# Kernel optimization log

Measured on AMD Instinct MI355X. Metric: run time of the kernel, lower is better.

## Reference

```python
import jax, jax.numpy as jnp
import numpy as np

B, T, I, E, H = 128, 64, 128, 256, 512


def setup_inputs() -> dict:
    key = jax.random.key(0)
    ks = jax.random.split(key, 8)
    inp = {}
    inp["input_data"] = jax.random.normal(ks[0], (B, T, I, E), dtype=jnp.float32)
    inp["news_W"] = jax.random.normal(ks[1], (1, E), dtype=jnp.float32) / np.sqrt(E)
    inp["news_b"] = jnp.zeros((1,), dtype=jnp.float32)
    inp["attn1_W"] = jax.random.normal(ks[2], (T, 2 * H), dtype=jnp.float32) / np.sqrt(2 * H)
    inp["attn1_b"] = jnp.zeros((T,), dtype=jnp.float32)
    inp["attn2_W"] = jax.random.normal(ks[3], (T, T), dtype=jnp.float32) / np.sqrt(T)
    inp["attn2_b"] = jnp.zeros((T,), dtype=jnp.float32)
    inp["attn3_W"] = jax.random.normal(ks[4], (1, T), dtype=jnp.float32) / np.sqrt(T)
    inp["attn3_b"] = jnp.zeros((1,), dtype=jnp.float32)
    inp["W_ih"] = jax.random.normal(ks[5], (4 * H, I), dtype=jnp.float32) / np.sqrt(I)
    inp["W_hh"] = jax.random.normal(ks[6], (4 * H, H), dtype=jnp.float32) / np.sqrt(H)
    inp["b_ih"] = jnp.zeros((4 * H,), dtype=jnp.float32)
    inp["b_hh"] = jnp.zeros((4 * H,), dtype=jnp.float32)
    return inp


def reference(input_data, news_W, news_b, attn1_W, attn1_b, attn2_W, attn2_b,
              attn3_W, attn3_b, W_ih, W_hh, b_ih, b_hh):
    # news_linear: [B,T,I,E] -> [B,T,I]
    x = jnp.einsum('btie,e->bti', input_data, news_W[0]) + news_b[0]
    # z2 is loop-invariant: attn2 on [B,I,T] -> [B,I,T]
    z2 = jnp.einsum('bit,st->bis', x.transpose(0, 2, 1), attn2_W) + attn2_b
    h0 = jnp.zeros((B, H), dtype=x.dtype)
    c0 = jnp.zeros((B, H), dtype=x.dtype)

    def step(carry, x_t):
        h, c = carry
        # hidden/cell repeated across I -> z1 identical for every driver i
        hc = jnp.concatenate([h, c], axis=-1)                   # [B,2H]
        z1 = hc @ attn1_W.T + attn1_b                           # [B,T]
        s = jnp.tanh(z1[:, None, :] + z2)                       # [B,I,T]
        z3 = jnp.einsum('bit,t->bi', s, attn3_W[0]) + attn3_b[0]  # [B,I]
        attn = jax.nn.softmax(z3, axis=1)                       # [B,I]
        w = attn * x_t                                          # [B,I]
        gates = w @ W_ih.T + h @ W_hh.T + b_ih + b_hh           # [B,4H]
        i_g, f_g, g_g, o_g = jnp.split(gates, 4, axis=-1)
        c_new = jax.nn.sigmoid(f_g) * c + jax.nn.sigmoid(i_g) * jnp.tanh(g_g)
        h_new = jax.nn.sigmoid(o_g) * jnp.tanh(c_new)
        return (h_new, c_new), h_new

    xs = x.transpose(1, 0, 2)                                   # [T,B,I]
    _, hs = jax.lax.scan(step, (h0, c0), xs)                    # [T,B,H]
    return hs.transpose(1, 0, 2)                                # [B,T,H]
```

## Files before the change

kernel.cpp:

```cpp
#include <hip/hip_runtime.h>
#include <cstdint>
#include <cstddef>

#define B 128
#define T 64
#define IDIM 128
#define E 256
#define H 512
#define NT 512

#define AT_STRIDE 34
#define AT_CH (128 * AT_STRIDE)

#define OFF_W   0
#define OFF_A   20480
#define OFF_HC  (OFF_A + 4 * AT_CH)
#define OFF_Z1  (OFF_HC + 1024)
#define OFF_RED (OFF_Z1 + 64)
#define OFF_BI  (OFF_RED + 128)
#define POOL_F  (OFF_BI + 32)

__device__ __forceinline__ float waveReduceSum(float v) {
    for (int off = 32; off > 0; off >>= 1) v += __shfl_xor(v, off, 64);
    return v;
}

__device__ __forceinline__ float fast_tanh(float v) {
    float a = fabsf(v);
    float e = __expf(-2.f * a);
    float r = (1.f - e) * __builtin_amdgcn_rcpf(1.f + e);
    return copysignf(r, v);
}

__device__ __forceinline__ float sigmoidf_(float x) {
    return 1.0f / (1.0f + __expf(-x));
}

__device__ __forceinline__ float aload(const float* p) {
    return __hip_atomic_load(p, __ATOMIC_RELAXED, __HIP_MEMORY_SCOPE_AGENT);
}
__device__ __forceinline__ void astore(float* p, float v) {
    __hip_atomic_store(p, v, __ATOMIC_RELAXED, __HIP_MEMORY_SCOPE_AGENT);
}

__device__ __forceinline__ float4 cload4(const float* p) {
    float4 v;
    asm volatile("global_load_dwordx4 %0, %1, off sc0 sc1" : "=v"(v) : "v"(p));
    return v;
}
__device__ __forceinline__ void waitvm0() {
    asm volatile("s_waitcnt vmcnt(0)" ::: "memory");
}

__global__ __launch_bounds__(256) void news_kernel(
    const float* __restrict__ in, const float* __restrict__ nW,
    const float* __restrict__ nb, float* __restrict__ x)
{
    int out_idx = blockIdx.x * 4 + (threadIdx.x >> 6);
    int lane = threadIdx.x & 63;
    const float4* src = (const float4*)(in + (size_t)out_idx * E);
    float4 a = src[lane];
    float4 wv = ((const float4*)nW)[lane];
    float s = a.x * wv.x + a.y * wv.y + a.z * wv.z + a.w * wv.w;
    s = waveReduceSum(s);
    if (lane == 0) x[out_idx] = s + nb[0];
}

__global__ __launch_bounds__(64) void z2_kernel(
    const float* __restrict__ x, const float* __restrict__ A2,
    const float* __restrict__ b2, float* __restrict__ z2)
{
    int b = blockIdx.x >> 7;
    int i = blockIdx.x & 127;
    int s = threadIdx.x;
    __shared__ float xs[T];
    xs[s] = x[((size_t)b * T + s) * IDIM + i];
    __syncthreads();
    float acc = b2[s];
    const float* arow = A2 + s * T;
#pragma unroll 8
    for (int tt = 0; tt < T; ++tt) acc += xs[tt] * arow[tt];
    z2[((size_t)b * IDIM + i) * T + s] = acc;
}

__device__ __forceinline__ void qarrive(int* cnt, int q, int ns, int ph) {
    __syncthreads();
    if (threadIdx.x == NT - 1) {
        asm volatile("s_waitcnt vmcnt(0) lgkmcnt(0)" ::: "memory");
        int* subp  = cnt + (q * 8 + (ns >> 3)) * 32;
        int* rootp = cnt + 1024 + q * 32;
        int old = __hip_atomic_fetch_add(subp, 1, __ATOMIC_RELAXED,
                                         __HIP_MEMORY_SCOPE_AGENT);
        if (old == ph * 8 - 1)
            __hip_atomic_fetch_add(rootp, 1, __ATOMIC_RELAXED,
                                   __HIP_MEMORY_SCOPE_AGENT);
    }
}
__device__ __forceinline__ void qwait(int* cnt, int q, int ph) {
    if (threadIdx.x == NT - 1) {
        int* rootp = cnt + 1024 + q * 32;
        int spins = 0;
        while (__hip_atomic_load(rootp, __ATOMIC_RELAXED,
                                 __HIP_MEMORY_SCOPE_AGENT) < ph * 8) {
            if (++spins > (1 << 16)) break;
        }
    }
    __syncthreads();
}

__global__ __launch_bounds__(NT, 1) void scan_kernel(
    const float* __restrict__ x, const float* __restrict__ z2,
    const float* __restrict__ A1, const float* __restrict__ b1,
    const float* __restrict__ a3w,
    const float* __restrict__ Wih, const float* __restrict__ Whh,
    const float* __restrict__ bih, const float* __restrict__ bhh,
    float* __restrict__ wbuf, float* __restrict__ hbuf, float* __restrict__ cbuf,
    int* __restrict__ cnt, float* __restrict__ out)
{
    __shared__ float pool[POOL_F];
    float* Wlds = pool + OFF_W;
    float* At4  = pool + OFF_A;
    float* hcs  = pool + OFF_HC;
    float* z1s  = pool + OFF_Z1;
    float* redl = pool + OFF_RED;
    float* blds = pool + OFF_BI;

    const int tid  = threadIdx.x;
    const int bid  = blockIdx.x;
    const int lane = tid & 63, wave = tid >> 6;
    const int q = bid >> 6, ns = bid & 63;
    const int b0 = q * 32, n0 = ns * 8;
    const int ab = b0 + (ns >> 1);
    const int par = ns & 1;
    const int jg = lane & 7, bg = lane >> 3;
    const int half = tid >> 8;
    const int sbh = (tid & 255) >> 3;
    const int st8 = tid & 7;

    for (int idx = tid; idx < 640 * 32; idx += NT) {
        int jj = idx / 640, k = idx - jj * 640;
        int j = (jj >> 3) * 512 + n0 + (jj & 7);
        Wlds[k * 32 + jj] = (k < 128) ? Wih[(size_t)j * 128 + k]
                                      : Whh[(size_t)j * 512 + (k - 128)];
    }
    if (tid < 32) {
        int j = (tid >> 3) * 512 + n0 + (tid & 7);
        blds[tid] = bih[j] + bhh[j];
    }

    float cown = 0.f;

    int ph = 0;
    for (int t = 0; t < T; ++t) {
        float4 hv[8];
        {
            const float* hrow = hbuf + (size_t)(b0 + sbh) * H + half * 256;
#pragma unroll
            for (int cc = 0; cc < 2; ++cc)
#pragma unroll
                for (int qq = 0; qq < 4; ++qq)
                    hv[cc * 4 + qq] = cload4(hrow + cc * 128 + (st8 + 8 * qq) * 4);
        }

        {
            hcs[tid]     = aload(hbuf + (size_t)ab * H + tid);
            hcs[H + tid] = aload(cbuf + (size_t)ab * H + tid);
            __syncthreads();
            for (int r = 0; r < 8; ++r) {
                int tt = r * 8 + wave;
                const float* row = A1 + (size_t)tt * (2 * H);
                float p = 0.f;
#pragma unroll
                for (int qq = 0; qq < 16; ++qq)
                    p += row[lane + qq * 64] * hcs[lane + qq * 64];
                p = waveReduceSum(p);
                if (lane == 0) z1s[tt] = p + b1[tt];
            }
            __syncthreads();
            int i = tid >> 2, qt = tid & 3;
            const float* z2r = z2 + ((size_t)ab * IDIM + i) * T + qt * 16;
            const float* z1p = z1s + qt * 16;
            const float* a3p = a3w + qt * 16;
            float accz = 0.f;
#pragma unroll
            for (int qq = 0; qq < 4; ++qq) {
                float4 zv  = *(const float4*)(z2r + qq * 4);
                float4 z1v = *(const float4*)(z1p + qq * 4);
                float4 a3v = *(const float4*)(a3p + qq * 4);
                accz += fast_tanh(z1v.x + zv.x) * a3v.x
                      + fast_tanh(z1v.y + zv.y) * a3v.y
                      + fast_tanh(z1v.z + zv.z) * a3v.z
                      + fast_tanh(z1v.w + zv.w) * a3v.w;
            }
            accz += __shfl_xor(accz, 1, 64);
            accz += __shfl_xor(accz, 2, 64);
            if (qt == 0) redl[i] = accz;
            __syncthreads();
            if (wave == 0) {
                float v0 = redl[lane], v1 = redl[lane + 64];
                float m = fmaxf(v0, v1);
                for (int off = 32; off > 0; off >>= 1)
                    m = fmaxf(m, __shfl_xor(m, off, 64));
                float e0 = __expf(v0 - m), e1 = __expf(v1 - m);
                float inv = 1.0f / waveReduceSum(e0 + e1);
                const float* xt = x + ((size_t)ab * T + t) * IDIM;
                if (par == 0)
                    astore(wbuf + ab * IDIM + lane,      e0 * inv * xt[lane]);
                else
                    astore(wbuf + ab * IDIM + lane + 64, e1 * inv * xt[lane + 64]);
            }
        }

        ++ph;
        qarrive(cnt, q, ns, ph);

        waitvm0();
        {
#pragma unroll
            for (int cc = 0; cc < 2; ++cc)
#pragma unroll
                for (int qq = 0; qq < 4; ++qq) {
                    float4 v = hv[cc * 4 + qq];
                    float* d = At4 + (half * 2 + cc) * AT_CH
                             + ((st8 + 8 * qq) * 4) * AT_STRIDE + sbh;
                    d[0] = v.x; d[AT_STRIDE] = v.y;
                    d[2 * AT_STRIDE] = v.z; d[3 * AT_STRIDE] = v.w;
                }
        }
        __syncthreads();

        float acc[4][4];
#pragma unroll
        for (int a_ = 0; a_ < 4; ++a_)
#pragma unroll
            for (int b_ = 0; b_ < 4; ++b_) acc[a_][b_] = 0.f;
        {
            const float* Ab = At4 + (wave >> 1) * AT_CH
                            + ((wave & 1) * 64) * AT_STRIDE + bg * 4;
            const float* Wb = Wlds + (size_t)(128 + wave * 64) * 32 + jg * 4;
#pragma unroll 8
            for (int i = 0; i < 64; ++i) {
                float4 wv = *(const float4*)(Wb + i * 32);
                float2 a01 = *(const float2*)(Ab + i * AT_STRIDE);
                float2 a23 = *(const float2*)(Ab + i * AT_STRIDE + 2);
                float av[4] = {a01.x, a01.y, a23.x, a23.y};
                const float wj[4] = {wv.x, wv.y, wv.z, wv.w};
#pragma unroll
                for (int a_ = 0; a_ < 4; ++a_)
#pragma unroll
                    for (int b_ = 0; b_ < 4; ++b_)
                        acc[a_][b_] += wj[a_] * av[b_];
            }
        }

        qwait(cnt, q, ph);

        {
            const float* wrow = wbuf + (size_t)(b0 + (tid >> 4)) * IDIM;
            float4 w0 = cload4(wrow + (tid & 15) * 4);
            float4 w1 = cload4(wrow + ((tid & 15) + 16) * 4);
            waitvm0();
            int sbw = tid >> 4, st16 = tid & 15;
            float* d0 = At4 + (st16 * 4) * AT_STRIDE + sbw;
            d0[0] = w0.x; d0[AT_STRIDE] = w0.y;
            d0[2 * AT_STRIDE] = w0.z; d0[3 * AT_STRIDE] = w0.w;
            float* d1 = At4 + ((st16 + 16) * 4) * AT_STRIDE + sbw;
            d1[0] = w1.x; d1[AT_STRIDE] = w1.y;
            d1[2 * AT_STRIDE] = w1.z; d1[3 * AT_STRIDE] = w1.w;
        }
        __syncthreads();
        {
            const float* Ab = At4 + (wave * 16) * AT_STRIDE + bg * 4;
            const float* Wb = Wlds + (size_t)(wave * 16) * 32 + jg * 4;
#pragma unroll
            for (int i = 0; i < 16; ++i) {
                float4 wv = *(const float4*)(Wb + i * 32);
                float2 a01 = *(const float2*)(Ab + i * AT_STRIDE);
                float2 a23 = *(const float2*)(Ab + i * AT_STRIDE + 2);
                float av[4] = {a01.x, a01.y, a23.x, a23.y};
                const float wj[4] = {wv.x, wv.y, wv.z, wv.w};
#pragma unroll
                for (int a_ = 0; a_ < 4; ++a_)
#pragma unroll
                    for (int b_ = 0; b_ < 4; ++b_)
                        acc[a_][b_] += wj[a_] * av[b_];
            }
        }

        float* red4 = At4 + AT_CH;
#pragma unroll
        for (int ji = 0; ji < 4; ++ji) {
            int r = jg * 4 + ji;
#pragma unroll
            for (int eb = 0; eb < 4; ++eb)
                red4[wave * 1056 + r * 33 + bg * 4 + ((eb + jg) & 3)] = acc[ji][eb];
        }
        __syncthreads();

        float* glds = At4;
        if (tid < 256) {
            int jj = tid >> 3, b8 = tid & 7;
            int rot = jj >> 2;
            float bias = blds[jj];
            float s[4] = {bias, bias, bias, bias};
#pragma unroll
            for (int w = 0; w < 8; ++w) {
                const float* rp = red4 + w * 1056 + jj * 33 + b8 * 4;
#pragma unroll
                for (int eb = 0; eb < 4; ++eb)
                    s[eb] += rp[(eb + rot) & 3];
            }
#pragma unroll
            for (int eb = 0; eb < 4; ++eb)
                glds[jj * 33 + b8 * 4 + eb] = s[eb];
        }
        __syncthreads();
        float hnew = 0.f;
        if (tid < 256) {
            int ub = tid >> 3, un = tid & 7;
            float ig = glds[(0 * 8 + un) * 33 + ub];
            float fg = glds[(1 * 8 + un) * 33 + ub];
            float gg = glds[(2 * 8 + un) * 33 + ub];
            float og = glds[(3 * 8 + un) * 33 + ub];
            int gb = b0 + ub, gn = n0 + un;
            float cnew = sigmoidf_(fg) * cown + sigmoidf_(ig) * tanhf(gg);
            hnew = sigmoidf_(og) * tanhf(cnew);
            cown = cnew;
            astore(cbuf + (size_t)gb * H + gn, cnew);
            astore(hbuf + (size_t)gb * H + gn, hnew);
        }

        ++ph;
        qarrive(cnt, q, ns, ph);
        if (tid < 256) {
            int gb = b0 + (tid >> 3), gn = n0 + (tid & 7);
            out[((size_t)gb * T + t) * H + gn] = hnew;
        }
        qwait(cnt, q, ph);
    }
}

extern "C" void kernel_launch(void* const* d_in, const int* in_sizes, int n_in,
                              void* d_out, int out_size, void* d_ws, size_t ws_size,
                              hipStream_t stream)
{
    const float* input  = (const float*)d_in[0];
    const float* news_W = (const float*)d_in[1];
    const float* news_b = (const float*)d_in[2];
    const float* A1     = (const float*)d_in[3];
    const float* b1     = (const float*)d_in[4];
    const float* A2     = (const float*)d_in[5];
    const float* b2     = (const float*)d_in[6];
    const float* a3w    = (const float*)d_in[7];
    const float* Wih    = (const float*)d_in[9];
    const float* Whh    = (const float*)d_in[10];
    const float* bih    = (const float*)d_in[11];
    const float* bhh    = (const float*)d_in[12];
    float* out = (float*)d_out;

    char* ws = (char*)d_ws;
    size_t off = 0;
    auto alloc = [&](size_t nelem) {
        float* p = (float*)(ws + off);
        off += ((nelem * 4 + 255) / 256) * 256;
        return p;
    };
    float* x    = alloc((size_t)B * T * IDIM);
    float* z2   = alloc((size_t)B * IDIM * T);
    float* wbuf = alloc((size_t)B * IDIM);
    float* hbuf = alloc((size_t)B * H);
    float* cbuf = alloc((size_t)B * H);
    int*   cnt  = (int*)alloc(2048);

    hipMemsetAsync(hbuf, 0, (size_t)B * H * 4, stream);
    hipMemsetAsync(cbuf, 0, (size_t)B * H * 4, stream);
    hipMemsetAsync(cnt, 0, 2048 * 4, stream);

    news_kernel<<<B * T * IDIM / 4, 256, 0, stream>>>(input, news_W, news_b, x);
    z2_kernel<<<B * IDIM, 64, 0, stream>>>(x, A2, b2, z2);
    scan_kernel<<<256, NT, 0, stream>>>(x, z2, A1, b1, a3w, Wih, Whh, bih, bhh,
                                        wbuf, hbuf, cbuf, cnt, out);
}
```

Baseline: 1.245 ms.

## Double block size to 1024 threads and split recurrent matvec across 16 waves

```diff
diff --git a/kernel.cpp b/kernel.cpp
--- a/kernel.cpp
+++ b/kernel.cpp
@@ -7,7 +7,7 @@
 #define IDIM 128
 #define E 256
 #define H 512
-#define NT 512
+#define NT 1024
 
 #define AT_STRIDE 34
 #define AT_CH (128 * AT_STRIDE)
@@ -134,7 +134,7 @@
     const int par = ns & 1;
     const int jg = lane & 7, bg = lane >> 3;
     const int half = tid >> 8;
-    const int sbh = (tid & 255) >> 3;
+    const int sbh = (tid >> 3) & 31;
     const int st8 = tid & 7;
 
     for (int idx = tid; idx < 640 * 32; idx += NT) {
@@ -152,22 +152,20 @@
 
     int ph = 0;
     for (int t = 0; t < T; ++t) {
-        float4 hv[8];
-        {
-            const float* hrow = hbuf + (size_t)(b0 + sbh) * H + half * 256;
-#pragma unroll
-            for (int cc = 0; cc < 2; ++cc)
-#pragma unroll
-                for (int qq = 0; qq < 4; ++qq)
-                    hv[cc * 4 + qq] = cload4(hrow + cc * 128 + (st8 + 8 * qq) * 4);
-        }
-
-        {
-            hcs[tid]     = aload(hbuf + (size_t)ab * H + tid);
-            hcs[H + tid] = aload(cbuf + (size_t)ab * H + tid);
+        float4 hv[4];
+        {
+            const float* hrow = hbuf + (size_t)(b0 + sbh) * H + half * 128;
+#pragma unroll
+            for (int qq = 0; qq < 4; ++qq)
+                hv[qq] = cload4(hrow + (st8 + 8 * qq) * 4);
+        }
+
+        {
+            hcs[tid] = (tid < H) ? aload(hbuf + (size_t)ab * H + tid)
+                                 : aload(cbuf + (size_t)ab * H + (tid - H));
             __syncthreads();
-            for (int r = 0; r < 8; ++r) {
-                int tt = r * 8 + wave;
+            for (int r = 0; r < 4; ++r) {
+                int tt = r * 16 + wave;
                 const float* row = A1 + (size_t)tt * (2 * H);
                 float p = 0.f;
 #pragma unroll
@@ -177,13 +175,13 @@
                 if (lane == 0) z1s[tt] = p + b1[tt];
             }
             __syncthreads();
-            int i = tid >> 2, qt = tid & 3;
-            const float* z2r = z2 + ((size_t)ab * IDIM + i) * T + qt * 16;
-            const float* z1p = z1s + qt * 16;
-            const float* a3p = a3w + qt * 16;
+            int i = tid >> 3, qt = tid & 7;
+            const float* z2r = z2 + ((size_t)ab * IDIM + i) * T + qt * 8;
+            const float* z1p = z1s + qt * 8;
+            const float* a3p = a3w + qt * 8;
             float accz = 0.f;
 #pragma unroll
-            for (int qq = 0; qq < 4; ++qq) {
+            for (int qq = 0; qq < 2; ++qq) {
                 float4 zv  = *(const float4*)(z2r + qq * 4);
                 float4 z1v = *(const float4*)(z1p + qq * 4);
                 float4 a3v = *(const float4*)(a3p + qq * 4);
@@ -194,6 +192,7 @@
             }
             accz += __shfl_xor(accz, 1, 64);
             accz += __shfl_xor(accz, 2, 64);
+            accz += __shfl_xor(accz, 4, 64);
             if (qt == 0) redl[i] = accz;
             __syncthreads();
             if (wave == 0) {
@@ -217,15 +216,13 @@
         waitvm0();
         {
 #pragma unroll
-            for (int cc = 0; cc < 2; ++cc)
-#pragma unroll
-                for (int qq = 0; qq < 4; ++qq) {
-                    float4 v = hv[cc * 4 + qq];
-                    float* d = At4 + (half * 2 + cc) * AT_CH
-                             + ((st8 + 8 * qq) * 4) * AT_STRIDE + sbh;
-                    d[0] = v.x; d[AT_STRIDE] = v.y;
-                    d[2 * AT_STRIDE] = v.z; d[3 * AT_STRIDE] = v.w;
-                }
+            for (int qq = 0; qq < 4; ++qq) {
+                float4 v = hv[qq];
+                float* d = At4 + half * AT_CH
+                         + ((st8 + 8 * qq) * 4) * AT_STRIDE + sbh;
+                d[0] = v.x; d[AT_STRIDE] = v.y;
+                d[2 * AT_STRIDE] = v.z; d[3 * AT_STRIDE] = v.w;
+            }
         }
         __syncthreads();
 
@@ -235,11 +232,11 @@
 #pragma unroll
             for (int b_ = 0; b_ < 4; ++b_) acc[a_][b_] = 0.f;
         {
-            const float* Ab = At4 + (wave >> 1) * AT_CH
-                            + ((wave & 1) * 64) * AT_STRIDE + bg * 4;
-            const float* Wb = Wlds + (size_t)(128 + wave * 64) * 32 + jg * 4;
+            const float* Ab = At4 + (wave >> 2) * AT_CH
+                            + ((wave & 3) * 32) * AT_STRIDE + bg * 4;
+            const float* Wb = Wlds + (size_t)(128 + wave * 32) * 32 + jg * 4;
 #pragma unroll 8
-            for (int i = 0; i < 64; ++i) {
+            for (int i = 0; i < 32; ++i) {
                 float4 wv = *(const float4*)(Wb + i * 32);
                 float2 a01 = *(const float2*)(Ab + i * AT_STRIDE);
                 float2 a23 = *(const float2*)(Ab + i * AT_STRIDE + 2);
@@ -256,24 +253,20 @@
         qwait(cnt, q, ph);
 
         {
-            const float* wrow = wbuf + (size_t)(b0 + (tid >> 4)) * IDIM;
-            float4 w0 = cload4(wrow + (tid & 15) * 4);
-            float4 w1 = cload4(wrow + ((tid & 15) + 16) * 4);
+            int st16 = tid & 15, sbw = (tid >> 4) & 31, kh = tid >> 9;
+            const float* wrow = wbuf + (size_t)(b0 + sbw) * IDIM;
+            float4 w0 = cload4(wrow + (st16 + kh * 16) * 4);
             waitvm0();
-            int sbw = tid >> 4, st16 = tid & 15;
-            float* d0 = At4 + (st16 * 4) * AT_STRIDE + sbw;
+            float* d0 = At4 + ((st16 + kh * 16) * 4) * AT_STRIDE + sbw;
             d0[0] = w0.x; d0[AT_STRIDE] = w0.y;
             d0[2 * AT_STRIDE] = w0.z; d0[3 * AT_STRIDE] = w0.w;
-            float* d1 = At4 + ((st16 + 16) * 4) * AT_STRIDE + sbw;
-            d1[0] = w1.x; d1[AT_STRIDE] = w1.y;
-            d1[2 * AT_STRIDE] = w1.z; d1[3 * AT_STRIDE] = w1.w;
-        }
-        __syncthreads();
-        {
-            const float* Ab = At4 + (wave * 16) * AT_STRIDE + bg * 4;
-            const float* Wb = Wlds + (size_t)(wave * 16) * 32 + jg * 4;
-#pragma unroll
-            for (int i = 0; i < 16; ++i) {
+        }
+        __syncthreads();
+        {
+            const float* Ab = At4 + (wave * 8) * AT_STRIDE + bg * 4;
+            const float* Wb = Wlds + (size_t)(wave * 8) * 32 + jg * 4;
+#pragma unroll
+            for (int i = 0; i < 8; ++i) {
                 float4 wv = *(const float4*)(Wb + i * 32);
                 float2 a01 = *(const float2*)(Ab + i * AT_STRIDE);
                 float2 a23 = *(const float2*)(Ab + i * AT_STRIDE + 2);
@@ -288,12 +281,26 @@
         }
 
         float* red4 = At4 + AT_CH;
-#pragma unroll
-        for (int ji = 0; ji < 4; ++ji) {
-            int r = jg * 4 + ji;
-#pragma unroll
-            for (int eb = 0; eb < 4; ++eb)
-                red4[wave * 1056 + r * 33 + bg * 4 + ((eb + jg) & 3)] = acc[ji][eb];
+        if (wave >= 8) {
+#pragma unroll
+            for (int ji = 0; ji < 4; ++ji) {
+                int r = jg * 4 + ji;
+#pragma unroll
+                for (int eb = 0; eb < 4; ++eb)
+                    red4[(wave - 8) * 1056 + r * 33 + bg * 4 + ((eb + jg) & 3)]
+                        = acc[ji][eb];
+            }
+        }
+        __syncthreads();
+        if (wave < 8) {
+#pragma unroll
+            for (int ji = 0; ji < 4; ++ji) {
+                int r = jg * 4 + ji;
+#pragma unroll
+                for (int eb = 0; eb < 4; ++eb)
+                    red4[wave * 1056 + r * 33 + bg * 4 + ((eb + jg) & 3)]
+                        += acc[ji][eb];
+            }
         }
         __syncthreads();
 
```

Result: slower. 1.439 ms (+15.6%).
